# Optimization experiments

Hardware: AMD Instinct MI355X
Metric: run time of the kernel (lower is better)

The kernel has to match this reference:

```python
import jax, jax.numpy as jnp
import numpy as np

N = 50000        # nodes
E = 800000       # edges (before self-loops)
NODE_IN = 128    # input feature dim
HID = 32         # per-head hidden dim
EPS = 1e-5       # batchnorm eps
NEG_SLOPE = 0.2  # GAT leaky-relu slope


def gat(x, src, dst, W, a_src, a_dst, b, heads, out_dim):
    """PyG-style GATConv (concat=True, self-loops added, eval-mode dropout)."""
    n = x.shape[0]
    h = (x @ W).reshape(n, heads, out_dim)                     # [n,H,D]
    loops = jnp.arange(n, dtype=src.dtype)
    s = jnp.concatenate([src, loops])                          # add self loops
    d = jnp.concatenate([dst, loops])
    e_src = jnp.einsum('nhd,hd->nh', h, a_src)                 # [n,H]
    e_dst = jnp.einsum('nhd,hd->nh', h, a_dst)
    alpha = jax.nn.leaky_relu(e_src[s] + e_dst[d], NEG_SLOPE)  # [E+n,H]
    m = jax.ops.segment_max(alpha, d, num_segments=n)          # segment softmax
    ex = jnp.exp(alpha - m[d])
    den = jax.ops.segment_sum(ex, d, num_segments=n)
    w = ex / den[d]                                            # [E+n,H]
    out = jax.ops.segment_sum(w[:, :, None] * h[s], d, num_segments=n)  # [n,H,D]
    return out.reshape(n, heads * out_dim) + b


def bn(x, gamma, beta):
    mu = x.mean(axis=0)
    var = x.var(axis=0)
    return (x - mu) * jax.lax.rsqrt(var + EPS) * gamma + beta


def setup_inputs() -> dict:
    key = jax.random.key(0)
    ks = jax.random.split(key, 20)
    nrm = lambda k, shape: jax.random.normal(k, shape, dtype=jnp.float32) * 0.1
    inp = {}
    inp['x'] = jax.random.normal(ks[0], (N, NODE_IN), dtype=jnp.float32)
    inp['edge_index'] = jax.random.randint(ks[1], (2, E), 0, N)
    inp['W1'] = nrm(ks[2], (NODE_IN, 4 * HID)); inp['as1'] = nrm(ks[3], (4, HID)); inp['ad1'] = nrm(ks[4], (4, HID)); inp['b1'] = jnp.zeros((4 * HID,))
    inp['g1'] = jnp.ones((4 * HID,)); inp['be1'] = jnp.zeros((4 * HID,))
    inp['W2'] = nrm(ks[5], (4 * HID, 4 * HID)); inp['as2'] = nrm(ks[6], (4, HID)); inp['ad2'] = nrm(ks[7], (4, HID)); inp['b2'] = jnp.zeros((4 * HID,))
    inp['g2'] = jnp.ones((4 * HID,)); inp['be2'] = jnp.zeros((4 * HID,))
    # encoder GAT3 (bottleneck): 128 -> 32, 1 head
    inp['W3'] = nrm(ks[8], (4 * HID, HID)); inp['as3'] = nrm(ks[9], (1, HID)); inp['ad3'] = nrm(ks[10], (1, HID)); inp['b3'] = jnp.zeros((HID,))
    # decoder GAT4: 32 -> 32, 1 head
    inp['W4'] = nrm(ks[11], (HID, HID)); inp['as4'] = nrm(ks[12], (1, HID)); inp['ad4'] = nrm(ks[13], (1, HID)); inp['b4'] = jnp.zeros((HID,))
    inp['g4'] = jnp.ones((HID,)); inp['be4'] = jnp.zeros((HID,))
    # decoder GAT5: 32 -> 128, 1 head
    inp['W5'] = nrm(ks[14], (HID, NODE_IN)); inp['as5'] = nrm(ks[15], (1, NODE_IN)); inp['ad5'] = nrm(ks[16], (1, NODE_IN)); inp['b5'] = jnp.zeros((NODE_IN,))
    return inp


def reference(x, edge_index, W1, as1, ad1, b1, g1, be1, W2, as2, ad2, b2, g2, be2,
              W3, as3, ad3, b3, W4, as4, ad4, b4, g4, be4, W5, as5, ad5, b5):
    src, dst = edge_index[0], edge_index[1]
    # encoder (dropout is identity in eval mode)
    h = jax.nn.relu(gat(x, src, dst, W1, as1, ad1, b1, heads=4, out_dim=HID))
    h = bn(h, g1, be1)
    h = jax.nn.relu(gat(h, src, dst, W2, as2, ad2, b2, heads=4, out_dim=HID))
    h = bn(h, g2, be2)
    h = jax.nn.relu(gat(h, src, dst, W3, as3, ad3, b3, heads=1, out_dim=HID))
    # decoder
    r = jax.nn.relu(gat(h, src, dst, W4, as4, ad4, b4, heads=1, out_dim=HID))
    r = jax.nn.relu(bn(r, g4, be4))
    return gat(r, src, dst, W5, as5, ad5, b5, heads=1, out_dim=NODE_IN)
```

## Files before the change

### kernel.cpp

```cpp
#include <hip/hip_runtime.h>
#include <math.h>

#define NNODES 50000
#define NEDGES 800000
#define BN_EPS 1e-5f
#define DEGC 128
#define NB 391
#define NPB 128
#define SCG 256
#define HWG 192
#define NSH 32

typedef unsigned int uint;
typedef unsigned short ushort;
typedef __attribute__((ext_vector_type(8))) short bf16x8;
typedef __attribute__((ext_vector_type(4))) float f32x4;

static __device__ __forceinline__ ushort f2bf(float f) {
    uint u = __float_as_uint(f);
    return (ushort)((u + 0x7fffu + ((u >> 16) & 1u)) >> 16);
}
static __device__ __forceinline__ float bfhi(ushort h) {
    return __uint_as_float((uint)h << 16);
}
static __device__ __forceinline__ float2 bf2f(uint v) {
    float2 r;
    r.x = __uint_as_float(v << 16);
    r.y = __uint_as_float(v & 0xffff0000u);
    return r;
}
static __device__ __forceinline__ void splitbf(float v, ushort& h, ushort& l) {
    h = f2bf(v);
    l = f2bf(v - bfhi(h));
}

__global__ __launch_bounds__(256) void histwt(const int* __restrict__ dst,
                                              int* __restrict__ bcnt,
                                              const float* __restrict__ W1,
                                              const float* __restrict__ W2,
                                              const float* __restrict__ W3,
                                              ushort* __restrict__ wt1h, ushort* __restrict__ wt1l,
                                              ushort* __restrict__ wt2h, ushort* __restrict__ wt2l,
                                              ushort* __restrict__ wt3h, ushort* __restrict__ wt3l) {
    if (blockIdx.x < HWG) {
        __shared__ int h[NB];
        for (int i = threadIdx.x; i < NB; i += 256) h[i] = 0;
        __syncthreads();
        for (int e = blockIdx.x * 256 + threadIdx.x; e < NEDGES; e += HWG * 256)
            atomicAdd(&h[dst[e] >> 7], 1);
        __syncthreads();
        for (int i = threadIdx.x; i < NB; i += 256)
            if (h[i]) atomicAdd(&bcnt[i], h[i]);
    } else {
        int idx = (blockIdx.x - HWG) * 256 + threadIdx.x;
        ushort h, l;
        if (idx < 16384) {
            int k = idx >> 7, c = idx & 127;
            splitbf(W1[idx], h, l);
            wt1h[c * 128 + k] = h; wt1l[c * 128 + k] = l;
        } else if (idx < 32768) {
            int i = idx - 16384;
            int k = i >> 7, c = i & 127;
            splitbf(W2[i], h, l);
            wt2h[c * 128 + k] = h; wt2l[c * 128 + k] = l;
        } else {
            int i = idx - 32768;
            int k = i >> 5, c = i & 31;
            splitbf(W3[i], h, l);
            wt3h[c * 128 + k] = h; wt3l[c * 128 + k] = l;
        }
    }
}

__global__ void bucket_scan(const int* __restrict__ bcnt, int* __restrict__ eoff,
                            int* __restrict__ boff, int* __restrict__ ecur,
                            int* __restrict__ off, const float* __restrict__ W5,
                            const float* __restrict__ as5, const float* __restrict__ ad5,
                            float* __restrict__ atl) {
    __shared__ int w1[8], w2[8];
    int t = threadIdx.x, lane = t & 63, wv = t >> 6;
    int v = (t < NB) ? bcnt[t] : 0;
    int nib = 0;
    if (t < NB) nib = (t == NB - 1) ? (NNODES - (NB - 1) * NPB) : NPB;
    int x1 = v, x2 = v + nib;
#pragma unroll
    for (int s = 1; s < 64; s <<= 1) {
        int t1 = __shfl_up(x1, s), t2 = __shfl_up(x2, s);
        if (lane >= s) { x1 += t1; x2 += t2; }
    }
    if (lane == 63) { w1[wv] = x1; w2[wv] = x2; }
    __syncthreads();
    if (wv == 0) {
        int a = (lane < 8) ? w1[lane] : 0, b = (lane < 8) ? w2[lane] : 0;
#pragma unroll
        for (int s = 1; s < 8; s <<= 1) {
            int ta = __shfl_up(a, s), tb = __shfl_up(b, s);
            if (lane >= s) { a += ta; b += tb; }
        }
        if (lane < 8) { w1[lane] = a; w2[lane] = b; }
    }
    __syncthreads();
    int p1 = (wv > 0) ? w1[wv - 1] : 0, p2 = (wv > 0) ? w2[wv - 1] : 0;
    x1 += p1; x2 += p2;
    if (t < NB) { eoff[t] = x1 - v; boff[t] = x2 - (v + nib); ecur[t] = 0; }
    if (t == NB - 1) { eoff[NB] = x1; boff[NB] = x2; off[NNODES] = x2; }
    if (t >= 448) {
        int idx = t - 448;
        int k = idx & 31;
        const float* a = (idx < 32) ? as5 : ad5;
        float s = 0.f;
        for (int f = 0; f < 128; ++f) s += W5[k * 128 + f] * a[f];
        atl[idx] = s;
    }
}

__global__ __launch_bounds__(256) void bucket_scatter(const int* __restrict__ src,
                                                      const int* __restrict__ dst,
                                                      const int* __restrict__ eoff,
                                                      int* __restrict__ ecur,
                                                      uint* __restrict__ ebuf) {
    __shared__ int lh[NB];
    __shared__ int lcur[NB];
    const int CH = (NEDGES + SCG - 1) / SCG;
    int c0 = blockIdx.x * CH;
    int c1 = min(c0 + CH, NEDGES);
    int t = threadIdx.x;
    for (int i = t; i < NB; i += 256) { lh[i] = 0; lcur[i] = 0; }
    __syncthreads();
    for (int e = c0 + t; e < c1; e += 256) atomicAdd(&lh[dst[e] >> 7], 1);
    __syncthreads();
    for (int i = t; i < NB; i += 256) {
        int c = lh[i];
        lh[i] = c ? (eoff[i] + atomicAdd(&ecur[i], c)) : 0;
    }
    __syncthreads();
    for (int e = c0 + t; e < c1; e += 256) {
        int d = dst[e];
        int bk = d >> 7;
        int p = lh[bk] + atomicAdd(&lcur[bk], 1);
        ebuf[p] = ((uint)(d & 127) << 16) | (uint)src[e];
    }
}

__global__ __launch_bounds__(256) void bucket_place(const uint* __restrict__ ebuf,
                                                    const int* __restrict__ eoff,
                                                    const int* __restrict__ boff,
                                                    int* __restrict__ off,
                                                    int* __restrict__ ssorted) {
    __shared__ int cnt[NPB];
    __shared__ int cur[NPB];
    __shared__ int wtot[2];
    int b = blockIdx.x;
    int nib = (b == NB - 1) ? (NNODES - (NB - 1) * NPB) : NPB;
    int t = threadIdx.x;
    for (int i = t; i < NPB; i += 256) { cnt[i] = 0; cur[i] = 0; }
    __syncthreads();
    int e0 = eoff[b], e1 = eoff[b + 1];
    for (int i = e0 + t; i < e1; i += 256) atomicAdd(&cnt[ebuf[i] >> 16], 1);
    __syncthreads();
    int lane = t & 63, wv = t >> 6;
    int deg = (t < nib) ? cnt[t] + 1 : 0;
    int x = deg;
#pragma unroll
    for (int s = 1; s < 64; s <<= 1) {
        int tv = __shfl_up(x, s);
        if (lane >= s) x += tv;
    }
    if (lane == 63 && wv < 2) wtot[wv] = x;
    __syncthreads();
    int excl = x - deg + ((wv == 1) ? wtot[0] : 0);
    if (t < nib) {
        int base = boff[b] + excl;
        off[b * NPB + t] = base;
        cnt[t] = excl;
        ssorted[base + deg - 1] = b * NPB + t;
    }
    __syncthreads();
    int bb = boff[b];
    for (int i = e0 + t; i < e1; i += 256) {
        uint v = ebuf[i];
        int ld = v >> 16;
        int pos = bb + cnt[ld] + atomicAdd(&cur[ld], 1);
        ssorted[pos] = (int)(v & 0xffffu);
    }
}

template <int KK, bool WBF, bool AFF>
__global__ __launch_bounds__(256) void mfma_mm(const float* __restrict__ X,
                                               const ushort* __restrict__ Wth,
                                               const ushort* __restrict__ Wtl,
                                               const float* __restrict__ bnsums,
                                               const float* __restrict__ bng,
                                               const float* __restrict__ bnbe,
                                               const float* __restrict__ av_s,
                                               const float* __restrict__ av_d,
                                               float* __restrict__ Of,
                                               ushort* __restrict__ Obf,
                                               float* __restrict__ es,
                                               float* __restrict__ ed,
                                               int N, float inv_n) {
    constexpr int KQ = KK / 32;
    constexpr int MI = WBF ? 4 : 1;
    __shared__ __align__(16) ushort sAh[64 * 136];
    __shared__ __align__(16) ushort sAl[64 * 136];
    __shared__ float sSc[128], sSh[128];
    int tid = threadIdx.x;
    int rowBase = blockIdx.x * 64;
    int lane = tid & 63, wv = tid >> 6;
    int lr = lane & 15, lq = lane >> 4;

    if constexpr (AFF) {
        if (tid < KK) {
            float su = 0.f, sq = 0.f;
#pragma unroll 4
            for (int sh = 0; sh < NSH; ++sh) {
                su += bnsums[sh * 256 + tid];
                sq += bnsums[sh * 256 + 128 + tid];
            }
            float mu = su * inv_n;
            float var = sq * inv_n - mu * mu;
            float s = bng[tid] * rsqrtf(var + BN_EPS);
            sSc[tid] = s;
            sSh[tid] = fmaf(-mu, s, bnbe[tid]);
        }
        __syncthreads();
    }

#pragma unroll
    for (int j = 0; j < 64 * KK / 4 / 256; ++j) {
        int idx = tid + j * 256;
        int row = idx / (KK / 4);
        int cq = idx - row * (KK / 4);
        int gr = rowBase + row;
        float4 v = make_float4(0.f, 0.f, 0.f, 0.f);
        if (gr < N) {
            v = *(const float4*)(X + (size_t)gr * KK + cq * 4);
            if constexpr (AFF) {
                int c = cq * 4;
                v.x = fmaf(v.x, sSc[c], sSh[c]);
                v.y = fmaf(v.y, sSc[c + 1], sSh[c + 1]);
                v.z = fmaf(v.z, sSc[c + 2], sSh[c + 2]);
                v.w = fmaf(v.w, sSc[c + 3], sSh[c + 3]);
            }
        }
        ushort h0, h1, h2, h3, l0, l1, l2, l3;
        splitbf(v.x, h0, l0); splitbf(v.y, h1, l1);
        splitbf(v.z, h2, l2); splitbf(v.w, h3, l3);
        uint2 ph, pl;
        ph.x = (uint)h0 | ((uint)h1 << 16);
        ph.y = (uint)h2 | ((uint)h3 << 16);
        pl.x = (uint)l0 | ((uint)l1 << 16);
        pl.y = (uint)l2 | ((uint)l3 << 16);
        *(uint2*)&sAh[row * 136 + cq * 4] = ph;
        *(uint2*)&sAl[row * 136 + cq * 4] = pl;
    }
    __syncthreads();

    const int mrow0 = WBF ? 0 : wv * 16;
    const int ncol0 = WBF ? wv * 32 : 0;
    f32x4 acc[MI][2];
#pragma unroll
    for (int mi = 0; mi < MI; ++mi)
#pragma unroll
        for (int ni = 0; ni < 2; ++ni) acc[mi][ni] = (f32x4){0.f, 0.f, 0.f, 0.f};

#pragma unroll
    for (int kq = 0; kq < KQ; ++kq) {
        int kb = kq * 32 + lq * 8;
        bf16x8 ah[MI], al[MI], bh[2], bl[2];
#pragma unroll
        for (int mi = 0; mi < MI; ++mi) {
            ah[mi] = *(const bf16x8*)&sAh[(mrow0 + 16 * mi + lr) * 136 + kb];
            al[mi] = *(const bf16x8*)&sAl[(mrow0 + 16 * mi + lr) * 136 + kb];
        }
#pragma unroll
        for (int ni = 0; ni < 2; ++ni) {
            size_t bo = (size_t)(ncol0 + 16 * ni + lr) * KK + kb;
            bh[ni] = *(const bf16x8*)(Wth + bo);
            bl[ni] = *(const bf16x8*)(Wtl + bo);
        }
#pragma unroll
        for (int mi = 0; mi < MI; ++mi)
#pragma unroll
            for (int ni = 0; ni < 2; ++ni) {
                acc[mi][ni] = __builtin_amdgcn_mfma_f32_16x16x32_bf16(
                    ah[mi], bh[ni], acc[mi][ni], 0, 0, 0);
                acc[mi][ni] = __builtin_amdgcn_mfma_f32_16x16x32_bf16(
                    al[mi], bh[ni], acc[mi][ni], 0, 0, 0);
                acc[mi][ni] = __builtin_amdgcn_mfma_f32_16x16x32_bf16(
                    ah[mi], bl[ni], acc[mi][ni], 0, 0, 0);
            }
    }

    {
        float as0 = av_s[ncol0 + lr], as1 = av_s[ncol0 + 16 + lr];
        float ad0 = av_d[ncol0 + lr], ad1 = av_d[ncol0 + 16 + lr];
#pragma unroll
        for (int mi = 0; mi < MI; ++mi)
#pragma unroll
            for (int r = 0; r < 4; ++r) {
                float ps = acc[mi][0][r] * as0 + acc[mi][1][r] * as1;
                float pd = acc[mi][0][r] * ad0 + acc[mi][1][r] * ad1;
#pragma unroll
                for (int s = 1; s < 16; s <<= 1) {
                    ps += __shfl_xor(ps, s);
                    pd += __shfl_xor(pd, s);
                }
                if (lr == 0) {
                    int gr = rowBase + mrow0 + 16 * mi + lq * 4 + r;
                    if (gr < N) {
                        if constexpr (WBF) {
                            es[(size_t)gr * 4 + wv] = ps;
                            ed[(size_t)gr * 4 + wv] = pd;
                        } else {
                            es[gr] = ps;
                            ed[gr] = pd;
                        }
                    }
                }
            }
    }
    __syncthreads();

    if constexpr (WBF) {
#pragma unroll
        for (int mi = 0; mi < MI; ++mi)
#pragma unroll
            for (int ni = 0; ni < 2; ++ni)
#pragma unroll
                for (int r = 0; r < 4; ++r)
                    sAh[(16 * mi + lq * 4 + r) * 136 + ncol0 + 16 * ni + lr] =
                        f2bf(acc[mi][ni][r]);
        __syncthreads();
        int row = tid >> 2, c0 = (tid & 3) * 32;
        int gr = rowBase + row;
        if (gr < N) {
            uint4 o0 = *(const uint4*)&sAh[row * 136 + c0];
            uint4 o1 = *(const uint4*)&sAh[row * 136 + c0 + 8];
            uint4 o2 = *(const uint4*)&sAh[row * 136 + c0 + 16];
            uint4 o3 = *(const uint4*)&sAh[row * 136 + c0 + 24];
            uint4* d4 = (uint4*)(Obf + (size_t)gr * 128 + c0);
            d4[0] = o0; d4[1] = o1; d4[2] = o2; d4[3] = o3;
        }
    } else {
        float* sOutF = (float*)sAh;
#pragma unroll
        for (int ni = 0; ni < 2; ++ni)
#pragma unroll
            for (int r = 0; r < 4; ++r)
                sOutF[(mrow0 + lq * 4 + r) * 36 + 16 * ni + lr] = acc[0][ni][r];
        __syncthreads();
        int row = tid >> 2, c0 = (tid & 3) * 8;
        int gr = rowBase + row;
        if (gr < N) {
            float4 v0 = *(const float4*)&sOutF[row * 36 + c0];
            float4 v1 = *(const float4*)&sOutF[row * 36 + c0 + 4];
            *(float4*)(Of + (size_t)gr * 32 + c0) = v0;
            *(float4*)(Of + (size_t)gr * 32 + c0 + 4) = v1;
        }
    }
}

__global__ __launch_bounds__(256) void node_agg_bf4(const int* __restrict__ off,
                                                    const int* __restrict__ ssorted,
                                                    const ushort* __restrict__ Hb,
                                                    const float* __restrict__ es,
                                                    const float* __restrict__ ed,
                                                    const float* __restrict__ bias,
                                                    float* __restrict__ outp,
                                                    float* __restrict__ sums) {
    __shared__ float lds_ex[4][DEGC * 4];
    __shared__ int lds_s[4][DEGC];
    __shared__ float red_v[4][128];
    __shared__ float red_q[4][128];
    int wib = threadIdx.x >> 6;
    int lane = threadIdx.x & 63;
    int d = blockIdx.x * 4 + wib;
    int beg = off[d], end = off[d + 1];
    int m = end - beg;

    int lh = lane & 3, le = lane >> 2;
    float edl = ed[(size_t)d * 4 + lh];
    float denp = 0.f;
    for (int base = 0; base < m; base += 16) {
        int e = base + le;
        if (e < m) {
            int s = ssorted[beg + e];
            if (lh == 0 && e < DEGC) lds_s[wib][e] = s;
            float a = es[(size_t)s * 4 + lh] + edl;
            a = a > 0.f ? a : 0.2f * a;
            float ex = __expf(a);
            denp += ex;
            if (e < DEGC) lds_ex[wib][e * 4 + lh] = ex;
        }
    }
#pragma unroll
    for (int sft = 4; sft < 64; sft <<= 1) denp += __shfl_xor(denp, sft);
    float inv = 1.f / denp;
    int mu = m < DEGC ? m : DEGC;
    for (int idx = lane; idx < mu * 4; idx += 64) lds_ex[wib][idx] *= inv;

    const uint* Hu = (const uint*)Hb;
    int head = lane >> 4;
    float inv2 = __shfl(inv, head);
    float edl2 = __shfl(edl, head);
    float acc0 = 0.f, acc1 = 0.f;
    int i = 0;
    for (; i + 8 <= mu; i += 8) {
        int sx[8];
        float wx[8];
        uint vx[8];
#pragma unroll
        for (int j = 0; j < 8; ++j) {
            sx[j] = lds_s[wib][i + j];
            wx[j] = lds_ex[wib][(i + j) * 4 + head];
        }
#pragma unroll
        for (int j = 0; j < 8; ++j) vx[j] = Hu[(size_t)sx[j] * 64 + lane];
#pragma unroll
        for (int j = 0; j < 8; ++j) {
            float2 f = bf2f(vx[j]);
            acc0 += wx[j] * f.x;
            acc1 += wx[j] * f.y;
        }
    }
    for (; i < mu; ++i) {
        int s = lds_s[wib][i];
        float w = lds_ex[wib][i * 4 + head];
        float2 f = bf2f(Hu[(size_t)s * 64 + lane]);
        acc0 += w * f.x;
        acc1 += w * f.y;
    }
    for (; i < m; ++i) {
        int s = ssorted[beg + i];
        float a = es[(size_t)s * 4 + head] + edl2;
        a = a > 0.f ? a : 0.2f * a;
        float w = __expf(a) * inv2;
        float2 f = bf2f(Hu[(size_t)s * 64 + lane]);
        acc0 += w * f.x;
        acc1 += w * f.y;
    }
    float v0 = fmaxf(acc0 + bias[2 * lane], 0.f);
    float v1 = fmaxf(acc1 + bias[2 * lane + 1], 0.f);
    *(float2*)(outp + (size_t)d * 128 + 2 * lane) = make_float2(v0, v1);

    red_v[wib][2 * lane] = v0;
    red_v[wib][2 * lane + 1] = v1;
    red_q[wib][2 * lane] = v0 * v0;
    red_q[wib][2 * lane + 1] = v1 * v1;
    __syncthreads();
    int t = threadIdx.x;
    int sh = (blockIdx.x & (NSH - 1)) * 256;
    if (t < 128) {
        float s = red_v[0][t] + red_v[1][t] + red_v[2][t] + red_v[3][t];
        atomicAdd(&sums[sh + t], s);
    } else {
        int u = t - 128;
        float q = red_q[0][u] + red_q[1][u] + red_q[2][u] + red_q[3][u];
        atomicAdd(&sums[sh + 128 + u], q);
    }
}

__global__ __launch_bounds__(256) void node_agg_f32s(const int* __restrict__ off,
                                                     const int* __restrict__ ssorted,
                                                     const float* __restrict__ Hb,
                                                     const float* __restrict__ es,
                                                     const float* __restrict__ ed,
                                                     const float* __restrict__ bias,
                                                     float* __restrict__ outp,
                                                     float* __restrict__ sums) {
    __shared__ float lds_ex[4][DEGC];
    __shared__ int lds_s[4][DEGC];
    __shared__ float red_v[4][32];
    __shared__ float red_q[4][32];
    int wib = threadIdx.x >> 6;
    int lane = threadIdx.x & 63;
    int d = blockIdx.x * 4 + wib;
    int beg = off[d], end = off[d + 1];
    int m = end - beg;

    float edv = ed[d];
    float denp = 0.f;
    for (int base = 0; base < m; base += 64) {
        int i = base + lane;
        if (i < m) {
            int s = ssorted[beg + i];
            if (i < DEGC) lds_s[wib][i] = s;
            float a = es[s] + edv;
            a = a > 0.f ? a : 0.2f * a;
            float ex = __expf(a);
            denp += ex;
            if (i < DEGC) lds_ex[wib][i] = ex;
        }
    }
#pragma unroll
    for (int sft = 1; sft < 64; sft <<= 1) denp += __shfl_xor(denp, sft);
    int mu = m < DEGC ? m : DEGC;
    float inv = 1.f / denp;
    for (int idx = lane; idx < mu; idx += 64) lds_ex[wib][idx] *= inv;

    int sub = lane >> 5, f = lane & 31;
    float acc = 0.f;
    int i = sub;
    for (; i + 14 < mu; i += 16) {
        int sx[8];
        float wx[8], hx[8];
#pragma unroll
        for (int j = 0; j < 8; ++j) {
            sx[j] = lds_s[wib][i + 2 * j];
            wx[j] = lds_ex[wib][i + 2 * j];
        }
#pragma unroll
        for (int j = 0; j < 8; ++j) hx[j] = Hb[(size_t)sx[j] * 32 + f];
#pragma unroll
        for (int j = 0; j < 8; ++j) acc += wx[j] * hx[j];
    }
    for (; i + 2 < mu; i += 4) {
        int s0 = lds_s[wib][i], s1 = lds_s[wib][i + 2];
        float w0 = lds_ex[wib][i], w1 = lds_ex[wib][i + 2];
        float h0 = Hb[(size_t)s0 * 32 + f], h1 = Hb[(size_t)s1 * 32 + f];
        acc += w0 * h0 + w1 * h1;
    }
    for (; i < mu; i += 2) {
        int s = lds_s[wib][i];
        acc += lds_ex[wib][i] * Hb[(size_t)s * 32 + f];
    }
    for (; i < m; i += 2) {
        int s = ssorted[beg + i];
        float a = es[s] + edv;
        a = a > 0.f ? a : 0.2f * a;
        acc += __expf(a) * inv * Hb[(size_t)s * 32 + f];
    }
    acc += __shfl_xor(acc, 32);
    float v = fmaxf(acc + bias[f], 0.f);
    if (sub == 0) {
        outp[(size_t)d * 32 + f] = v;
        red_v[wib][f] = v;
        red_q[wib][f] = v * v;
    }
    __syncthreads();
    int t = threadIdx.x;
    int sh = (blockIdx.x & (NSH - 1)) * 64;
    if (t < 32) {
        float s = red_v[0][t] + red_v[1][t] + red_v[2][t] + red_v[3][t];
        atomicAdd(&sums[sh + t], s);
    } else if (t < 64) {
        int u = t - 32;
        float q = red_q[0][u] + red_q[1][u] + red_q[2][u] + red_q[3][u];
        atomicAdd(&sums[sh + 32 + u], q);
    }
}

__global__ __launch_bounds__(256) void agg_mm32(const int* __restrict__ off,
                                                const int* __restrict__ ssorted,
                                                const float* __restrict__ Hb,
                                                const float* __restrict__ es,
                                                const float* __restrict__ ed,
                                                const float* __restrict__ bias,
                                                const float* __restrict__ W4,
                                                const float* __restrict__ as4,
                                                const float* __restrict__ ad4,
                                                float* __restrict__ outp,
                                                float* __restrict__ es_o,
                                                float* __restrict__ ed_o) {
    __shared__ float lds_ex[4][DEGC];
    __shared__ int lds_s[4][DEGC];
    __shared__ float sW[32][32];
    __shared__ float sV[4][32];
    for (int i = threadIdx.x; i < 1024; i += 256) sW[i >> 5][i & 31] = W4[i];
    __syncthreads();
    int wib = threadIdx.x >> 6;
    int lane = threadIdx.x & 63;
    int d = blockIdx.x * 4 + wib;
    int beg = off[d], end = off[d + 1];
    int m = end - beg;

    float edv = ed[d];
    float denp = 0.f;
    for (int base = 0; base < m; base += 64) {
        int i = base + lane;
        if (i < m) {
            int s = ssorted[beg + i];
            if (i < DEGC) lds_s[wib][i] = s;
            float a = es[s] + edv;
            a = a > 0.f ? a : 0.2f * a;
            float ex = __expf(a);
            denp += ex;
            if (i < DEGC) lds_ex[wib][i] = ex;
        }
    }
#pragma unroll
    for (int sft = 1; sft < 64; sft <<= 1) denp += __shfl_xor(denp, sft);
    int mu = m < DEGC ? m : DEGC;
    float inv = 1.f / denp;
    for (int idx = lane; idx < mu; idx += 64) lds_ex[wib][idx] *= inv;

    int sub = lane >> 5, f = lane & 31;
    float acc = 0.f;
    int i = sub;
    for (; i + 14 < mu; i += 16) {
        int sx[8];
        float wx[8], hx[8];
#pragma unroll
        for (int j = 0; j < 8; ++j) {
            sx[j] = lds_s[wib][i + 2 * j];
            wx[j] = lds_ex[wib][i + 2 * j];
        }
#pragma unroll
        for (int j = 0; j < 8; ++j) hx[j] = Hb[(size_t)sx[j] * 32 + f];
#pragma unroll
        for (int j = 0; j < 8; ++j) acc += wx[j] * hx[j];
    }
    for (; i + 2 < mu; i += 4) {
        int s0 = lds_s[wib][i], s1 = lds_s[wib][i + 2];
        float w0 = lds_ex[wib][i], w1 = lds_ex[wib][i + 2];
        float h0 = Hb[(size_t)s0 * 32 + f], h1 = Hb[(size_t)s1 * 32 + f];
        acc += w0 * h0 + w1 * h1;
    }
    for (; i < mu; i += 2) {
        int s = lds_s[wib][i];
        acc += lds_ex[wib][i] * Hb[(size_t)s * 32 + f];
    }
    for (; i < m; i += 2) {
        int s = ssorted[beg + i];
        float a = es[s] + edv;
        a = a > 0.f ? a : 0.2f * a;
        acc += __expf(a) * inv * Hb[(size_t)s * 32 + f];
    }
    acc += __shfl_xor(acc, 32);
    float v = fmaxf(acc + bias[f], 0.f);
    if (sub == 0) sV[wib][f] = v;
    float o = 0.f;
#pragma unroll
    for (int f2 = 0; f2 < 32; ++f2) o = fmaf(sV[wib][f2], sW[f2][f], o);
    if (sub == 0) outp[(size_t)d * 32 + f] = o;
    float ps = o * as4[f], pd = o * ad4[f];
#pragma unroll
    for (int sft = 1; sft < 32; sft <<= 1) { ps += __shfl_xor(ps, sft); pd += __shfl_xor(pd, sft); }
    if (lane == 0) { es_o[d] = ps; ed_o[d] = pd; }
}

__global__ __launch_bounds__(256) void agg_mm128(const int* __restrict__ off,
                                                 const int* __restrict__ ssorted,
                                                 const float* __restrict__ Hb,
                                                 const float* __restrict__ es,
                                                 const float* __restrict__ ed,
                                                 const float* __restrict__ W5,
                                                 const float* __restrict__ b5,
                                                 float* __restrict__ outp) {
    __shared__ float lds_ex[4][DEGC];
    __shared__ int lds_s[4][DEGC];
    __shared__ float sW[32][128];
    __shared__ float sV[4][32];
    for (int i = threadIdx.x; i < 4096; i += 256) ((float*)sW)[i] = W5[i];
    __syncthreads();
    int wib = threadIdx.x >> 6;
    int lane = threadIdx.x & 63;
    int d = blockIdx.x * 4 + wib;
    int beg = off[d], end = off[d + 1];
    int m = end - beg;

    float edv = ed[d];
    float denp = 0.f;
    for (int base = 0; base < m; base += 64) {
        int i = base + lane;
        if (i < m) {
            int s = ssorted[beg + i];
            if (i < DEGC) lds_s[wib][i] = s;
            float a = es[s] + edv;
            a = a > 0.f ? a : 0.2f * a;
            float ex = __expf(a);
            denp += ex;
            if (i < DEGC) lds_ex[wib][i] = ex;
        }
    }
#pragma unroll
    for (int sft = 1; sft < 64; sft <<= 1) denp += __shfl_xor(denp, sft);
    int mu = m < DEGC ? m : DEGC;
    float inv = 1.f / denp;
    for (int idx = lane; idx < mu; idx += 64) lds_ex[wib][idx] *= inv;

    int sub = lane >> 5, f = lane & 31;
    float acc = 0.f;
    int i = sub;
    for (; i + 14 < mu; i += 16) {
        int sx[8];
        float wx[8], hx[8];
#pragma unroll
        for (int j = 0; j < 8; ++j) {
            sx[j] = lds_s[wib][i + 2 * j];
            wx[j] = lds_ex[wib][i + 2 * j];
        }
#pragma unroll
        for (int j = 0; j < 8; ++j) hx[j] = Hb[(size_t)sx[j] * 32 + f];
#pragma unroll
        for (int j = 0; j < 8; ++j) acc += wx[j] * hx[j];
    }
    for (; i + 2 < mu; i += 4) {
        int s0 = lds_s[wib][i], s1 = lds_s[wib][i + 2];
        float w0 = lds_ex[wib][i], w1 = lds_ex[wib][i + 2];
        float h0 = Hb[(size_t)s0 * 32 + f], h1 = Hb[(size_t)s1 * 32 + f];
        acc += w0 * h0 + w1 * h1;
    }
    for (; i < mu; i += 2) {
        int s = lds_s[wib][i];
        acc += lds_ex[wib][i] * Hb[(size_t)s * 32 + f];
    }
    for (; i < m; i += 2) {
        int s = ssorted[beg + i];
        float a = es[s] + edv;
        a = a > 0.f ? a : 0.2f * a;
        acc += __expf(a) * inv * Hb[(size_t)s * 32 + f];
    }
    acc += __shfl_xor(acc, 32);
    if (sub == 0) sV[wib][f] = acc;
    float o0 = 0.f, o1 = 0.f;
    int c = lane * 2;
#pragma unroll
    for (int f2 = 0; f2 < 32; ++f2) {
        float vv = sV[wib][f2];
        float2 w2 = *(const float2*)&sW[f2][c];
        o0 = fmaf(vv, w2.x, o0);
        o1 = fmaf(vv, w2.y, o1);
    }
    float2 rb = *(const float2*)&b5[c];
    *(float2*)(outp + (size_t)d * 128 + c) = make_float2(o0 + rb.x, o1 + rb.y);
}

__global__ __launch_bounds__(256) void bn_relu_attn(const float* __restrict__ y,
                                                    const float* __restrict__ sums,
                                                    const float* __restrict__ g,
                                                    const float* __restrict__ be,
                                                    const float* __restrict__ atl,
                                                    float* __restrict__ o,
                                                    float* __restrict__ es,
                                                    float* __restrict__ ed) {
    __shared__ float ssc[32], ssh[32];
    int t = threadIdx.x;
    if (t < 32) {
        float su = 0.f, sq = 0.f;
#pragma unroll 4
        for (int sh = 0; sh < NSH; ++sh) { su += sums[sh * 64 + t]; sq += sums[sh * 64 + 32 + t]; }
        float mu = su / (float)NNODES;
        float var = sq / (float)NNODES - mu * mu;
        float sc = rsqrtf(var + BN_EPS) * g[t];
        ssc[t] = sc;
        ssh[t] = fmaf(-mu, sc, be[t]);
    }
    __syncthreads();
    int r = blockIdx.x * 8 + (t >> 5);
    int f = t & 31;
    float v = fmaxf(fmaf(y[(size_t)r * 32 + f], ssc[f], ssh[f]), 0.f);
    o[(size_t)r * 32 + f] = v;
    float ps = v * atl[f], pd = v * atl[32 + f];
#pragma unroll
    for (int s = 1; s < 32; s <<= 1) { ps += __shfl_xor(ps, s); pd += __shfl_xor(pd, s); }
    if (f == 0) { es[r] = ps; ed[r] = pd; }
}

extern "C" void kernel_launch(void* const* d_in, const int* in_sizes, int n_in, void* d_out,
                              int out_size, void* d_ws, size_t ws_size, hipStream_t stream) {
    const int N = NNODES, E = NEDGES;
    const float* x = (const float*)d_in[0];
    const int* ei = (const int*)d_in[1];
    const int* src = ei;
    const int* dst = ei + E;
    const float* W1 = (const float*)d_in[2];
    const float* as1 = (const float*)d_in[3];
    const float* ad1 = (const float*)d_in[4];
    const float* b1 = (const float*)d_in[5];
    const float* g1 = (const float*)d_in[6];
    const float* be1 = (const float*)d_in[7];
    const float* W2 = (const float*)d_in[8];
    const float* as2 = (const float*)d_in[9];
    const float* ad2 = (const float*)d_in[10];
    const float* b2 = (const float*)d_in[11];
    const float* g2 = (const float*)d_in[12];
    const float* be2 = (const float*)d_in[13];
    const float* W3 = (const float*)d_in[14];
    const float* as3 = (const float*)d_in[15];
    const float* ad3 = (const float*)d_in[16];
    const float* b3 = (const float*)d_in[17];
    const float* W4 = (const float*)d_in[18];
    const float* as4 = (const float*)d_in[19];
    const float* ad4 = (const float*)d_in[20];
    const float* b4 = (const float*)d_in[21];
    const float* g4 = (const float*)d_in[22];
    const float* be4 = (const float*)d_in[23];
    const float* W5 = (const float*)d_in[24];
    const float* as5 = (const float*)d_in[25];
    const float* ad5 = (const float*)d_in[26];
    const float* b5 = (const float*)d_in[27];
    float* out = (float*)d_out;

    float* ws = (float*)d_ws;
    float* bufAf = ws;
    float* bufB = ws + (size_t)N * 128;
    ushort* bufAbf = (ushort*)(ws + (size_t)2 * N * 128);
    uint* ebuf = (uint*)bufAbf;
    float* esA = ws + (size_t)2 * N * 128 + (size_t)N * 64;
    float* edA = esA + (size_t)N * 4;
    float* esB = edA + (size_t)N * 4;
    float* edB = esB + (size_t)N * 4;
    float* sums = edB + (size_t)N * 4;
    float* sumsA = sums;
    float* sumsB = sums + (size_t)NSH * 256;
    float* sums32 = sums + (size_t)2 * NSH * 256;
    int* bcnt = (int*)(sums + (size_t)NSH * 576);
    int* eoff = bcnt + NB;
    int* boff = eoff + NB + 1;
    int* ecur = boff + NB + 1;
    float* atl = (float*)(ecur + NB);
    int* off = (int*)(atl + 64);
    int* ssorted = off + N + 1;
    size_t wtoff = (((size_t)((ssorted + E + N) - (int*)ws)) + 3) & ~(size_t)3;
    ushort* wt1h = (ushort*)((int*)ws + wtoff);
    ushort* wt1l = wt1h + 16384;
    ushort* wt2h = wt1l + 16384;
    ushort* wt2l = wt2h + 16384;
    ushort* wt3h = wt2l + 16384;
    ushort* wt3l = wt3h + 4096;

    const int TB = 256;
    const int gAgg = N / 4;
    const int gMM = (N + 63) / 64;
    const float inv_n = 1.f / (float)N;

    hipMemsetAsync(sums, 0, ((size_t)NSH * 576 + NB) * sizeof(float), stream);

    histwt<<<HWG + 144, TB, 0, stream>>>(dst, bcnt, W1, W2, W3, wt1h, wt1l, wt2h, wt2l,
                                         wt3h, wt3l);
    bucket_scan<<<1, 512, 0, stream>>>(bcnt, eoff, boff, ecur, off, W5, as5, ad5, atl);
    bucket_scatter<<<SCG, TB, 0, stream>>>(src, dst, eoff, ecur, ebuf);
    bucket_place<<<NB, TB, 0, stream>>>(ebuf, eoff, boff, off, ssorted);

    mfma_mm<128, true, false><<<gMM, TB, 0, stream>>>(
        x, wt1h, wt1l, nullptr, nullptr, nullptr, as1, ad1, nullptr, bufAbf, esA, edA,
        N, inv_n);
    node_agg_bf4<<<gAgg, TB, 0, stream>>>(off, ssorted, bufAbf, esA, edA, b1, bufB, sumsA);

    mfma_mm<128, true, true><<<gMM, TB, 0, stream>>>(
        bufB, wt2h, wt2l, sumsA, g1, be1, as2, ad2, nullptr, bufAbf, esB, edB,
        N, inv_n);
    node_agg_bf4<<<gAgg, TB, 0, stream>>>(off, ssorted, bufAbf, esB, edB, b2, bufB, sumsB);

    mfma_mm<128, false, true><<<gMM, TB, 0, stream>>>(
        bufB, wt3h, wt3l, sumsB, g2, be2, as3, ad3, bufAf, nullptr, esA, edA,
        N, inv_n);

    agg_mm32<<<gAgg, TB, 0, stream>>>(off, ssorted, bufAf, esA, edA, b3, W4, as4, ad4,
                                      bufB, esB, edB);

    node_agg_f32s<<<gAgg, TB, 0, stream>>>(off, ssorted, bufB, esB, edB, b4, bufAf, sums32);
    bn_relu_attn<<<N / 8, TB, 0, stream>>>(bufAf, sums32, g4, be4, atl, bufB, esA, edA);

    agg_mm128<<<gAgg, TB, 0, stream>>>(off, ssorted, bufB, esA, edA, W5, b5, out);
}
```

Measured before the change: 448.8 us.

## Fuse layer-1 GEMM into edge scatter launch and use half-wave per node in 32-wide aggregations

```diff
diff --git a/kernel.cpp b/kernel.cpp
--- a/kernel.cpp
+++ b/kernel.cpp
@@ -114,31 +114,143 @@
     }
 }
 
-__global__ __launch_bounds__(256) void bucket_scatter(const int* __restrict__ src,
-                                                      const int* __restrict__ dst,
-                                                      const int* __restrict__ eoff,
-                                                      int* __restrict__ ecur,
-                                                      uint* __restrict__ ebuf) {
+__global__ __launch_bounds__(256) void scatter_mm(const int* __restrict__ src,
+                                                  const int* __restrict__ dst,
+                                                  const int* __restrict__ eoff,
+                                                  int* __restrict__ ecur,
+                                                  uint* __restrict__ ebuf,
+                                                  const float* __restrict__ X,
+                                                  const ushort* __restrict__ Wth,
+                                                  const ushort* __restrict__ Wtl,
+                                                  const float* __restrict__ av_s,
+                                                  const float* __restrict__ av_d,
+                                                  ushort* __restrict__ Obf,
+                                                  float* __restrict__ es,
+                                                  float* __restrict__ ed, int N) {
     __shared__ int lh[NB];
     __shared__ int lcur[NB];
-    const int CH = (NEDGES + SCG - 1) / SCG;
-    int c0 = blockIdx.x * CH;
-    int c1 = min(c0 + CH, NEDGES);
-    int t = threadIdx.x;
-    for (int i = t; i < NB; i += 256) { lh[i] = 0; lcur[i] = 0; }
-    __syncthreads();
-    for (int e = c0 + t; e < c1; e += 256) atomicAdd(&lh[dst[e] >> 7], 1);
-    __syncthreads();
-    for (int i = t; i < NB; i += 256) {
-        int c = lh[i];
-        lh[i] = c ? (eoff[i] + atomicAdd(&ecur[i], c)) : 0;
-    }
-    __syncthreads();
-    for (int e = c0 + t; e < c1; e += 256) {
-        int d = dst[e];
-        int bk = d >> 7;
-        int p = lh[bk] + atomicAdd(&lcur[bk], 1);
-        ebuf[p] = ((uint)(d & 127) << 16) | (uint)src[e];
+    __shared__ __align__(16) ushort sAh[64 * 136];
+    __shared__ __align__(16) ushort sAl[64 * 136];
+    int tid = threadIdx.x;
+    if (blockIdx.x < SCG) {
+        const int CH = (NEDGES + SCG - 1) / SCG;
+        int c0 = blockIdx.x * CH;
+        int c1 = min(c0 + CH, NEDGES);
+        for (int i = tid; i < NB; i += 256) { lh[i] = 0; lcur[i] = 0; }
+        __syncthreads();
+        for (int e = c0 + tid; e < c1; e += 256) atomicAdd(&lh[dst[e] >> 7], 1);
+        __syncthreads();
+        for (int i = tid; i < NB; i += 256) {
+            int c = lh[i];
+            lh[i] = c ? (eoff[i] + atomicAdd(&ecur[i], c)) : 0;
+        }
+        __syncthreads();
+        for (int e = c0 + tid; e < c1; e += 256) {
+            int d = dst[e];
+            int bk = d >> 7;
+            int p = lh[bk] + atomicAdd(&lcur[bk], 1);
+            ebuf[p] = ((uint)(d & 127) << 16) | (uint)src[e];
+        }
+        return;
+    }
+    int rowBase = (int)(blockIdx.x - SCG) * 64;
+    int lane = tid & 63, wv = tid >> 6;
+    int lr = lane & 15, lq = lane >> 4;
+#pragma unroll
+    for (int j = 0; j < 8; ++j) {
+        int idx = tid + j * 256;
+        int row = idx >> 5;
+        int cq = idx & 31;
+        int gr = rowBase + row;
+        float4 v = make_float4(0.f, 0.f, 0.f, 0.f);
+        if (gr < N) v = *(const float4*)(X + (size_t)gr * 128 + cq * 4);
+        ushort h0, h1, h2, h3, l0, l1, l2, l3;
+        splitbf(v.x, h0, l0); splitbf(v.y, h1, l1);
+        splitbf(v.z, h2, l2); splitbf(v.w, h3, l3);
+        uint2 ph, pl;
+        ph.x = (uint)h0 | ((uint)h1 << 16);
+        ph.y = (uint)h2 | ((uint)h3 << 16);
+        pl.x = (uint)l0 | ((uint)l1 << 16);
+        pl.y = (uint)l2 | ((uint)l3 << 16);
+        *(uint2*)&sAh[row * 136 + cq * 4] = ph;
+        *(uint2*)&sAl[row * 136 + cq * 4] = pl;
+    }
+    __syncthreads();
+    const int ncol0 = wv * 32;
+    f32x4 acc[4][2];
+#pragma unroll
+    for (int mi = 0; mi < 4; ++mi)
+#pragma unroll
+        for (int ni = 0; ni < 2; ++ni) acc[mi][ni] = (f32x4){0.f, 0.f, 0.f, 0.f};
+#pragma unroll
+    for (int kq = 0; kq < 4; ++kq) {
+        int kb = kq * 32 + lq * 8;
+        bf16x8 ah[4], al[4], bh[2], bl[2];
+#pragma unroll
+        for (int mi = 0; mi < 4; ++mi) {
+            ah[mi] = *(const bf16x8*)&sAh[(16 * mi + lr) * 136 + kb];
+            al[mi] = *(const bf16x8*)&sAl[(16 * mi + lr) * 136 + kb];
+        }
+#pragma unroll
+        for (int ni = 0; ni < 2; ++ni) {
+            size_t bo = (size_t)(ncol0 + 16 * ni + lr) * 128 + kb;
+            bh[ni] = *(const bf16x8*)(Wth + bo);
+            bl[ni] = *(const bf16x8*)(Wtl + bo);
+        }
+#pragma unroll
+        for (int mi = 0; mi < 4; ++mi)
+#pragma unroll
+            for (int ni = 0; ni < 2; ++ni) {
+                acc[mi][ni] = __builtin_amdgcn_mfma_f32_16x16x32_bf16(
+                    ah[mi], bh[ni], acc[mi][ni], 0, 0, 0);
+                acc[mi][ni] = __builtin_amdgcn_mfma_f32_16x16x32_bf16(
+                    al[mi], bh[ni], acc[mi][ni], 0, 0, 0);
+                acc[mi][ni] = __builtin_amdgcn_mfma_f32_16x16x32_bf16(
+                    ah[mi], bl[ni], acc[mi][ni], 0, 0, 0);
+            }
+    }
+    {
+        float as0 = av_s[ncol0 + lr], as1 = av_s[ncol0 + 16 + lr];
+        float ad0 = av_d[ncol0 + lr], ad1 = av_d[ncol0 + 16 + lr];
+#pragma unroll
+        for (int mi = 0; mi < 4; ++mi)
+#pragma unroll
+            for (int r = 0; r < 4; ++r) {
+                float ps = acc[mi][0][r] * as0 + acc[mi][1][r] * as1;
+                float pd = acc[mi][0][r] * ad0 + acc[mi][1][r] * ad1;
+#pragma unroll
+                for (int s = 1; s < 16; s <<= 1) {
+                    ps += __shfl_xor(ps, s);
+                    pd += __shfl_xor(pd, s);
+                }
+                if (lr == 0) {
+                    int gr = rowBase + 16 * mi + lq * 4 + r;
+                    if (gr < N) {
+                        es[(size_t)gr * 4 + wv] = ps;
+                        ed[(size_t)gr * 4 + wv] = pd;
+                    }
+                }
+            }
+    }
+    __syncthreads();
+#pragma unroll
+    for (int mi = 0; mi < 4; ++mi)
+#pragma unroll
+        for (int ni = 0; ni < 2; ++ni)
+#pragma unroll
+            for (int r = 0; r < 4; ++r)
+                sAh[(16 * mi + lq * 4 + r) * 136 + ncol0 + 16 * ni + lr] =
+                    f2bf(acc[mi][ni][r]);
+    __syncthreads();
+    int row = tid >> 2, c0 = (tid & 3) * 32;
+    int gr = rowBase + row;
+    if (gr < N) {
+        uint4 o0 = *(const uint4*)&sAh[row * 136 + c0];
+        uint4 o1 = *(const uint4*)&sAh[row * 136 + c0 + 8];
+        uint4 o2 = *(const uint4*)&sAh[row * 136 + c0 + 16];
+        uint4 o3 = *(const uint4*)&sAh[row * 136 + c0 + 24];
+        uint4* d4 = (uint4*)(Obf + (size_t)gr * 128 + c0);
+        d4[0] = o0; d4[1] = o1; d4[2] = o2; d4[3] = o3;
     }
 }
 
@@ -469,84 +581,77 @@
                                                      const float* __restrict__ bias,
                                                      float* __restrict__ outp,
                                                      float* __restrict__ sums) {
-    __shared__ float lds_ex[4][DEGC];
-    __shared__ int lds_s[4][DEGC];
-    __shared__ float red_v[4][32];
-    __shared__ float red_q[4][32];
-    int wib = threadIdx.x >> 6;
-    int lane = threadIdx.x & 63;
-    int d = blockIdx.x * 4 + wib;
+    __shared__ float lds_ex[8][DEGC];
+    __shared__ int lds_s[8][DEGC];
+    __shared__ float red_v[8][32];
+    __shared__ float red_q[8][32];
+    int tid = threadIdx.x;
+    int wib = tid >> 6, lane = tid & 63;
+    int grp = lane >> 5, g = lane & 31;
+    int nn = wib * 2 + grp;
+    int d = blockIdx.x * 8 + nn;
     int beg = off[d], end = off[d + 1];
     int m = end - beg;
 
     float edv = ed[d];
     float denp = 0.f;
-    for (int base = 0; base < m; base += 64) {
-        int i = base + lane;
-        if (i < m) {
-            int s = ssorted[beg + i];
-            if (i < DEGC) lds_s[wib][i] = s;
+    for (int base = 0; base < m; base += 32) {
+        int e = base + g;
+        if (e < m) {
+            int s = ssorted[beg + e];
+            if (e < DEGC) lds_s[nn][e] = s;
             float a = es[s] + edv;
             a = a > 0.f ? a : 0.2f * a;
             float ex = __expf(a);
             denp += ex;
-            if (i < DEGC) lds_ex[wib][i] = ex;
-        }
-    }
-#pragma unroll
-    for (int sft = 1; sft < 64; sft <<= 1) denp += __shfl_xor(denp, sft);
+            if (e < DEGC) lds_ex[nn][e] = ex;
+        }
+    }
+#pragma unroll
+    for (int sft = 1; sft < 32; sft <<= 1) denp += __shfl_xor(denp, sft);
     int mu = m < DEGC ? m : DEGC;
     float inv = 1.f / denp;
-    for (int idx = lane; idx < mu; idx += 64) lds_ex[wib][idx] *= inv;
-
-    int sub = lane >> 5, f = lane & 31;
+    for (int idx = g; idx < mu; idx += 32) lds_ex[nn][idx] *= inv;
+
+    int f = g;
     float acc = 0.f;
-    int i = sub;
-    for (; i + 14 < mu; i += 16) {
+    int i = 0;
+    for (; i + 8 <= mu; i += 8) {
         int sx[8];
         float wx[8], hx[8];
 #pragma unroll
-        for (int j = 0; j < 8; ++j) {
-            sx[j] = lds_s[wib][i + 2 * j];
-            wx[j] = lds_ex[wib][i + 2 * j];
-        }
+        for (int j = 0; j < 8; ++j) { sx[j] = lds_s[nn][i + j]; wx[j] = lds_ex[nn][i + j]; }
 #pragma unroll
         for (int j = 0; j < 8; ++j) hx[j] = Hb[(size_t)sx[j] * 32 + f];
 #pragma unroll
         for (int j = 0; j < 8; ++j) acc += wx[j] * hx[j];
     }
-    for (; i + 2 < mu; i += 4) {
-        int s0 = lds_s[wib][i], s1 = lds_s[wib][i + 2];
-        float w0 = lds_ex[wib][i], w1 = lds_ex[wib][i + 2];
-        float h0 = Hb[(size_t)s0 * 32 + f], h1 = Hb[(size_t)s1 * 32 + f];
-        acc += w0 * h0 + w1 * h1;
-    }
-    for (; i < mu; i += 2) {
-        int s = lds_s[wib][i];
-        acc += lds_ex[wib][i] * Hb[(size_t)s * 32 + f];
-    }
-    for (; i < m; i += 2) {
+    for (; i < mu; ++i) {
+        int s = lds_s[nn][i];
+        acc += lds_ex[nn][i] * Hb[(size_t)s * 32 + f];
+    }
+    for (; i < m; ++i) {
         int s = ssorted[beg + i];
         float a = es[s] + edv;
         a = a > 0.f ? a : 0.2f * a;
         acc += __expf(a) * inv * Hb[(size_t)s * 32 + f];
     }
-    acc += __shfl_xor(acc, 32);
     float v = fmaxf(acc + bias[f], 0.f);
-    if (sub == 0) {
-        outp[(size_t)d * 32 + f] = v;
-        red_v[wib][f] = v;
-        red_q[wib][f] = v * v;
-    }
-    __syncthreads();
-    int t = threadIdx.x;
+    outp[(size_t)d * 32 + f] = v;
+    red_v[nn][f] = v;
+    red_q[nn][f] = v * v;
+    __syncthreads();
     int sh = (blockIdx.x & (NSH - 1)) * 64;
-    if (t < 32) {
-        float s = red_v[0][t] + red_v[1][t] + red_v[2][t] + red_v[3][t];
-        atomicAdd(&sums[sh + t], s);
-    } else if (t < 64) {
-        int u = t - 32;
-        float q = red_q[0][u] + red_q[1][u] + red_q[2][u] + red_q[3][u];
+    if (tid < 32) {
+        float s = 0.f;
+#pragma unroll
+        for (int k = 0; k < 8; ++k) s += red_v[k][tid];
+        atomicAdd(&sums[sh + tid], s);
+    } else if (tid < 64) {
+        int u = tid - 32;
+        float q = 0.f;
+#pragma unroll
+        for (int k = 0; k < 8; ++k) q += red_q[k][u];
         atomicAdd(&sums[sh + 32 + u], q);
     }
 }
@@ -563,81 +668,73 @@
                                                 float* __restrict__ outp,
                                                 float* __restrict__ es_o,
                                                 float* __restrict__ ed_o) {
-    __shared__ float lds_ex[4][DEGC];
-    __shared__ int lds_s[4][DEGC];
+    __shared__ float lds_ex[8][DEGC];
+    __shared__ int lds_s[8][DEGC];
     __shared__ float sW[32][32];
-    __shared__ float sV[4][32];
-    for (int i = threadIdx.x; i < 1024; i += 256) sW[i >> 5][i & 31] = W4[i];
-    __syncthreads();
-    int wib = threadIdx.x >> 6;
-    int lane = threadIdx.x & 63;
-    int d = blockIdx.x * 4 + wib;
+    __shared__ float sV[8][32];
+    int tid = threadIdx.x;
+    for (int i = tid; i < 1024; i += 256) sW[i >> 5][i & 31] = W4[i];
+    __syncthreads();
+    int wib = tid >> 6, lane = tid & 63;
+    int grp = lane >> 5, g = lane & 31;
+    int nn = wib * 2 + grp;
+    int d = blockIdx.x * 8 + nn;
     int beg = off[d], end = off[d + 1];
     int m = end - beg;
 
     float edv = ed[d];
     float denp = 0.f;
-    for (int base = 0; base < m; base += 64) {
-        int i = base + lane;
-        if (i < m) {
-            int s = ssorted[beg + i];
-            if (i < DEGC) lds_s[wib][i] = s;
+    for (int base = 0; base < m; base += 32) {
+        int e = base + g;
+        if (e < m) {
+            int s = ssorted[beg + e];
+            if (e < DEGC) lds_s[nn][e] = s;
             float a = es[s] + edv;
             a = a > 0.f ? a : 0.2f * a;
             float ex = __expf(a);
             denp += ex;
-            if (i < DEGC) lds_ex[wib][i] = ex;
-        }
-    }
-#pragma unroll
-    for (int sft = 1; sft < 64; sft <<= 1) denp += __shfl_xor(denp, sft);
+            if (e < DEGC) lds_ex[nn][e] = ex;
+        }
+    }
+#pragma unroll
+    for (int sft = 1; sft < 32; sft <<= 1) denp += __shfl_xor(denp, sft);
     int mu = m < DEGC ? m : DEGC;
     float inv = 1.f / denp;
-    for (int idx = lane; idx < mu; idx += 64) lds_ex[wib][idx] *= inv;
-
-    int sub = lane >> 5, f = lane & 31;
+    for (int idx = g; idx < mu; idx += 32) lds_ex[nn][idx] *= inv;
+
+    int f = g;
     float acc = 0.f;
-    int i = sub;
-    for (; i + 14 < mu; i += 16) {
+    int i = 0;
+    for (; i + 8 <= mu; i += 8) {
         int sx[8];
         float wx[8], hx[8];
 #pragma unroll
-        for (int j = 0; j < 8; ++j) {
-            sx[j] = lds_s[wib][i + 2 * j];
-            wx[j] = lds_ex[wib][i + 2 * j];
-        }
+        for (int j = 0; j < 8; ++j) { sx[j] = lds_s[nn][i + j]; wx[j] = lds_ex[nn][i + j]; }
 #pragma unroll
         for (int j = 0; j < 8; ++j) hx[j] = Hb[(size_t)sx[j] * 32 + f];
 #pragma unroll
         for (int j = 0; j < 8; ++j) acc += wx[j] * hx[j];
     }
-    for (; i + 2 < mu; i += 4) {
-        int s0 = lds_s[wib][i], s1 = lds_s[wib][i + 2];
-        float w0 = lds_ex[wib][i], w1 = lds_ex[wib][i + 2];
-        float h0 = Hb[(size_t)s0 * 32 + f], h1 = Hb[(size_t)s1 * 32 + f];
-        acc += w0 * h0 + w1 * h1;
-    }
-    for (; i < mu; i += 2) {
-        int s = lds_s[wib][i];
-        acc += lds_ex[wib][i] * Hb[(size_t)s * 32 + f];
-    }
-    for (; i < m; i += 2) {
+    for (; i < mu; ++i) {
+        int s = lds_s[nn][i];
+        acc += lds_ex[nn][i] * Hb[(size_t)s * 32 + f];
+    }
+    for (; i < m; ++i) {
         int s = ssorted[beg + i];
         float a = es[s] + edv;
         a = a > 0.f ? a : 0.2f * a;
         acc += __expf(a) * inv * Hb[(size_t)s * 32 + f];
     }
-    acc += __shfl_xor(acc, 32);
     float v = fmaxf(acc + bias[f], 0.f);
-    if (sub == 0) sV[wib][f] = v;
+    sV[nn][f] = v;
     float o = 0.f;
 #pragma unroll
-    for (int f2 = 0; f2 < 32; ++f2) o = fmaf(sV[wib][f2], sW[f2][f], o);
-    if (sub == 0) outp[(size_t)d * 32 + f] = o;
+    for (int f2 = 0; f2 < 32; ++f2) o = fmaf(sV[nn][f2], sW[f2][f], o);
+    outp[(size_t)d * 32 + f] = o;
     float ps = o * as4[f], pd = o * ad4[f];
 #pragma unroll
     for (int sft = 1; sft < 32; sft <<= 1) { ps += __shfl_xor(ps, sft); pd += __shfl_xor(pd, sft); }
-    if (lane == 0) { es_o[d] = ps; ed_o[d] = pd; }
+    if (g == 0) { es_o[d] = ps; ed_o[d] = pd; }
 }
 
 __global__ __launch_bounds__(256) void agg_mm128(const int* __restrict__ off,
@@ -648,83 +745,78 @@
                                                  const float* __restrict__ W5,
                                                  const float* __restrict__ b5,
                                                  float* __restrict__ outp) {
-    __shared__ float lds_ex[4][DEGC];
-    __shared__ int lds_s[4][DEGC];
+    __shared__ float lds_ex[8][DEGC];
+    __shared__ int lds_s[8][DEGC];
     __shared__ float sW[32][128];
-    __shared__ float sV[4][32];
-    for (int i = threadIdx.x; i < 4096; i += 256) ((float*)sW)[i] = W5[i];
-    __syncthreads();
-    int wib = threadIdx.x >> 6;
-    int lane = threadIdx.x & 63;
-    int d = blockIdx.x * 4 + wib;
+    __shared__ float sV[8][32];
+    int tid = threadIdx.x;
+    for (int i = tid; i < 4096; i += 256) ((float*)sW)[i] = W5[i];
+    __syncthreads();
+    int wib = tid >> 6, lane = tid & 63;
+    int grp = lane >> 5, g = lane & 31;
+    int nn = wib * 2 + grp;
+    int d = blockIdx.x * 8 + nn;
     int beg = off[d], end = off[d + 1];
     int m = end - beg;
 
     float edv = ed[d];
     float denp = 0.f;
-    for (int base = 0; base < m; base += 64) {
-        int i = base + lane;
-        if (i < m) {
-            int s = ssorted[beg + i];
-            if (i < DEGC) lds_s[wib][i] = s;
+    for (int base = 0; base < m; base += 32) {
+        int e = base + g;
+        if (e < m) {
+            int s = ssorted[beg + e];
+            if (e < DEGC) lds_s[nn][e] = s;
             float a = es[s] + edv;
             a = a > 0.f ? a : 0.2f * a;
             float ex = __expf(a);
             denp += ex;
-            if (i < DEGC) lds_ex[wib][i] = ex;
-        }
-    }
-#pragma unroll
-    for (int sft = 1; sft < 64; sft <<= 1) denp += __shfl_xor(denp, sft);
+            if (e < DEGC) lds_ex[nn][e] = ex;
+        }
+    }
+#pragma unroll
+    for (int sft = 1; sft < 32; sft <<= 1) denp += __shfl_xor(denp, sft);
     int mu = m < DEGC ? m : DEGC;
     float inv = 1.f / denp;
-    for (int idx = lane; idx < mu; idx += 64) lds_ex[wib][idx] *= inv;
-
-    int sub = lane >> 5, f = lane & 31;
+    for (int idx = g; idx < mu; idx += 32) lds_ex[nn][idx] *= inv;
+
+    int f = g;
     float acc = 0.f;
-    int i = sub;
-    for (; i + 14 < mu; i += 16) {
+    int i = 0;
+    for (; i + 8 <= mu; i += 8) {
         int sx[8];
         float wx[8], hx[8];
 #pragma unroll
-        for (int j = 0; j < 8; ++j) {
-            sx[j] = lds_s[wib][i + 2 * j];
-            wx[j] = lds_ex[wib][i + 2 * j];
-        }
+        for (int j = 0; j < 8; ++j) { sx[j] = lds_s[nn][i + j]; wx[j] = lds_ex[nn][i + j]; }
 #pragma unroll
         for (int j = 0; j < 8; ++j) hx[j] = Hb[(size_t)sx[j] * 32 + f];
 #pragma unroll
         for (int j = 0; j < 8; ++j) acc += wx[j] * hx[j];
     }
-    for (; i + 2 < mu; i += 4) {
-        int s0 = lds_s[wib][i], s1 = lds_s[wib][i + 2];
-        float w0 = lds_ex[wib][i], w1 = lds_ex[wib][i + 2];
-        float h0 = Hb[(size_t)s0 * 32 + f], h1 = Hb[(size_t)s1 * 32 + f];
-        acc += w0 * h0 + w1 * h1;
-    }
-    for (; i < mu; i += 2) {
-        int s = lds_s[wib][i];
-        acc += lds_ex[wib][i] * Hb[(size_t)s * 32 + f];
-    }
-    for (; i < m; i += 2) {
+    for (; i < mu; ++i) {
+        int s = lds_s[nn][i];
+        acc += lds_ex[nn][i] * Hb[(size_t)s * 32 + f];
+    }
+    for (; i < m; ++i) {
         int s = ssorted[beg + i];
         float a = es[s] + edv;
         a = a > 0.f ? a : 0.2f * a;
         acc += __expf(a) * inv * Hb[(size_t)s * 32 + f];
     }
-    acc += __shfl_xor(acc, 32);
-    if (sub == 0) sV[wib][f] = acc;
-    float o0 = 0.f, o1 = 0.f;
-    int c = lane * 2;
+    sV[nn][f] = acc;
+    float o0 = 0.f, o1 = 0.f, o2 = 0.f, o3 = 0.f;
+    int c = g * 4;
 #pragma unroll
     for (int f2 = 0; f2 < 32; ++f2) {
-        float vv = sV[wib][f2];
-        float2 w2 = *(const float2*)&sW[f2][c];
-        o0 = fmaf(vv, w2.x, o0);
-        o1 = fmaf(vv, w2.y, o1);
-    }
-    float2 rb = *(const float2*)&b5[c];
-    *(float2*)(outp + (size_t)d * 128 + c) = make_float2(o0 + rb.x, o1 + rb.y);
+        float vv = sV[nn][f2];
+        float4 w4 = *(const float4*)&sW[f2][c];
+        o0 = fmaf(vv, w4.x, o0);
+        o1 = fmaf(vv, w4.y, o1);
+        o2 = fmaf(vv, w4.z, o2);
+        o3 = fmaf(vv, w4.w, o3);
+    }
+    float4 rb = *(const float4*)&b5[c];
+    *(float4*)(outp + (size_t)d * 128 + c) =
+        make_float4(o0 + rb.x, o1 + rb.y, o2 + rb.z, o3 + rb.w);
 }
 
 __global__ __launch_bounds__(256) void bn_relu_attn(const float* __restrict__ y,
@@ -797,7 +889,7 @@
     float* bufAf = ws;
     float* bufB = ws + (size_t)N * 128;
     ushort* bufAbf = (ushort*)(ws + (size_t)2 * N * 128);
-    uint* ebuf = (uint*)bufAbf;
+    uint* ebuf = (uint*)bufAf;
     float* esA = ws + (size_t)2 * N * 128 + (size_t)N * 64;
     float* edA = esA + (size_t)N * 4;
     float* esB = edA + (size_t)N * 4;
@@ -823,6 +915,7 @@
 
     const int TB = 256;
     const int gAgg = N / 4;
+    const int gAgg2 = N / 8;
     const int gMM = (N + 63) / 64;
     const float inv_n = 1.f / (float)N;
 
@@ -831,12 +924,11 @@
     histwt<<<HWG + 144, TB, 0, stream>>>(dst, bcnt, W1, W2, W3, wt1h, wt1l, wt2h, wt2l,
                                          wt3h, wt3l);
     bucket_scan<<<1, 512, 0, stream>>>(bcnt, eoff, boff, ecur, off, W5, as5, ad5, atl);
-    bucket_scatter<<<SCG, TB, 0, stream>>>(src, dst, eoff, ecur, ebuf);
+
+    scatter_mm<<<SCG + gMM, TB, 0, stream>>>(src, dst, eoff, ecur, ebuf, x, wt1h, wt1l,
+                                             as1, ad1, bufAbf, esA, edA, N);
     bucket_place<<<NB, TB, 0, stream>>>(ebuf, eoff, boff, off, ssorted);
 
-    mfma_mm<128, true, false><<<gMM, TB, 0, stream>>>(
-        x, wt1h, wt1l, nullptr, nullptr, nullptr, as1, ad1, nullptr, bufAbf, esA, edA,
-        N, inv_n);
     node_agg_bf4<<<gAgg, TB, 0, stream>>>(off, ssorted, bufAbf, esA, edA, b1, bufB, sumsA);
 
     mfma_mm<128, true, true><<<gMM, TB, 0, stream>>>(
@@ -848,11 +940,11 @@
         bufB, wt3h, wt3l, sumsB, g2, be2, as3, ad3, bufAf, nullptr, esA, edA,
         N, inv_n);
 
-    agg_mm32<<<gAgg, TB, 0, stream>>>(off, ssorted, bufAf, esA, edA, b3, W4, as4, ad4,
-                                      bufB, esB, edB);
-
-    node_agg_f32s<<<gAgg, TB, 0, stream>>>(off, ssorted, bufB, esB, edB, b4, bufAf, sums32);
+    agg_mm32<<<gAgg2, TB, 0, stream>>>(off, ssorted, bufAf, esA, edA, b3, W4, as4, ad4,
+                                       bufB, esB, edB);
+
+    node_agg_f32s<<<gAgg2, TB, 0, stream>>>(off, ssorted, bufB, esB, edB, b4, bufAf, sums32);
     bn_relu_attn<<<N / 8, TB, 0, stream>>>(bufAf, sums32, g4, be4, atl, bufB, esA, edA);
 
-    agg_mm128<<<gAgg, TB, 0, stream>>>(off, ssorted, bufB, esA, edA, W5, b5, out);
-}
+    agg_mm128<<<gAgg2, TB, 0, stream>>>(off, ssorted, bufB, esA, edA, W5, b5, out);
+}
```

Result: faster. 412.8 us (-8.0%).
